# Performance work log

Hardware: AMD Instinct MI355X
Metric: run time of the kernel (lower is better)

Reference implementation:

```python
import jax, jax.numpy as jnp
import numpy as np

C, T, D = 32, 768, 100      # n_countries, n_times, n_ages (=n_features)
H = 5                        # attention heads (EncoderLayer default)
HID_GCN = 60                 # GCN hidden features
FFN = 64                     # feed_forward_dim
NPRED = 10                   # n_predictions
LHID = 200                   # hid_linear_part_dim
NL = 3                       # encoder layers


def setup_inputs() -> dict:
    key = jax.random.key(0)
    ks = jax.random.split(key, 24)
    s = 0.05
    rn = lambda k, shp: jax.random.normal(k, shp, jnp.float32) * s
    return {
        "X": jax.random.normal(ks[0], (C, T, D), jnp.float32),
        "A": jax.random.uniform(ks[1], (C, C), jnp.float32),
        # GCN params
        "gcn_w1": rn(ks[2], (D, HID_GCN)),
        "gcn_b1": rn(ks[3], (HID_GCN,)),
        "gcn_w2": rn(ks[4], (HID_GCN, D)),
        "gcn_b2": rn(ks[5], (D,)),
        # 3 stacked encoder layers
        "enc_wq": rn(ks[6], (NL, H, D, D)),
        "enc_wk": rn(ks[7], (NL, H, D, D)),
        "enc_wv": rn(ks[8], (NL, H, D, D)),
        "enc_wm": rn(ks[9], (NL, H * D, D)),
        "enc_f1w": rn(ks[10], (NL, D, FFN)),
        "enc_f1b": rn(ks[11], (NL, FFN)),
        "enc_f2w": rn(ks[12], (NL, FFN, D)),
        "enc_f2b": rn(ks[13], (NL, D)),
        "enc_ln1g": jnp.ones((NL, D), jnp.float32),
        "enc_ln1b": jnp.zeros((NL, D), jnp.float32),
        "enc_ln2g": jnp.ones((NL, D), jnp.float32),
        "enc_ln2b": jnp.zeros((NL, D), jnp.float32),
        "lin1_w": rn(ks[14], (D, LHID)),
        "lin1_b": rn(ks[15], (LHID,)),
        "lin2_w": rn(ks[16], (LHID, D)),
        "lin2_b": rn(ks[17], (D,)),
    }


def _layer_norm(x, g, b, eps=1e-5):
    m = x.mean(-1, keepdims=True)
    v = ((x - m) ** 2).mean(-1, keepdims=True)
    return (x - m) / jnp.sqrt(v + eps) * g + b


def _encoder_layer(x, wq, wk, wv, wm, f1w, f1b, f2w, f2b, g1, b1, g2, b2):
    # x: [C, T, D]; wq/wk/wv: [H, D, D]
    Q = jnp.einsum('ctd,hde->chte', x, wq)
    K = jnp.einsum('ctd,hde->chte', x, wk)
    V = jnp.einsum('ctd,hde->chte', x, wv)
    scores = jnp.einsum('chte,chse->chts', Q, K) / jnp.sqrt(jnp.float32(D))
    attn = jax.nn.softmax(scores, axis=-1)
    out = jnp.einsum('chts,chse->chte', attn, V)        # [C,H,T,D]
    out = out.transpose(0, 2, 1, 3).reshape(x.shape[0], x.shape[1], H * D)
    x = _layer_norm(x + out @ wm, g1, b1)
    ffn = jax.nn.relu(x @ f1w + f1b) @ f2w + f2b
    return _layer_norm(x + ffn, g2, b2)


def reference(X, A, gcn_w1, gcn_b1, gcn_w2, gcn_b2,
              enc_wq, enc_wk, enc_wv, enc_wm,
              enc_f1w, enc_f1b, enc_f2w, enc_f2b,
              enc_ln1g, enc_ln1b, enc_ln2g, enc_ln2b,
              lin1_w, lin1_b, lin2_w, lin2_b):
    n = A.shape[0]
    adj = A + jnp.eye(n, dtype=A.dtype)
    adj_hat = adj / adj.sum(-1, keepdims=True)
    # GCN layer 1
    h = jnp.einsum('ij,jta->ita', adj_hat, X)
    h = jnp.einsum('ita,ao->ito', h, gcn_w1) + gcn_b1
    h = jax.nn.relu(h)
    # GCN layer 2
    h = jnp.einsum('ij,jta->ita', adj_hat, h)
    h = jnp.einsum('ita,ao->ito', h, gcn_w2) + gcn_b2
    # 3 encoder layers (fixed structural loop)
    for l in range(NL):
        h = _encoder_layer(h, enc_wq[l], enc_wk[l], enc_wv[l], enc_wm[l],
                           enc_f1w[l], enc_f1b[l], enc_f2w[l], enc_f2b[l],
                           enc_ln1g[l], enc_ln1b[l], enc_ln2g[l], enc_ln2b[l])
    last = h[:, -1, :]  # [C, D]
    def step(carry, _):
        p = (carry @ lin1_w + lin1_b) @ lin2_w + lin2_b
        return p, p
    _, preds = jax.lax.scan(step, last, None, length=NPRED)  # [NPRED, C, D]
    return preds.transpose(1, 0, 2)  # [C, NPRED, D]
```

## Files before the change

### kernel.cpp

```cpp
#include <hip/hip_runtime.h>


#define ROWS 24576

#define OFF_ADJ   0L
#define OFF_X0    1024L
#define OFF_X1    (OFF_X0 + 2457600L)
#define OFF_XROW  (OFF_X1 + 3932160L)
#define OFF_XT    (OFF_XROW + 1572864L)
#define OFF_WBF   (OFF_XT + 1572864L)
#define OFF_MHT   (OFF_WBF + 6291456L)
#define OFF_USTT  (OFF_MHT + 122880L)
#define OFF_MP    (OFF_USTT + 98304L)
#define OFF_C0    (OFF_MP + 10000L)
#define OFF_F1WT  (OFF_C0 + 128L)
#define OFF_F2WT  (OFF_F1WT + 12288L)
#define OFF_GW1T  (OFF_F2WT + 10752L)
#define OFF_GW2T  (OFF_GW1T + 4096L)

typedef __attribute__((ext_vector_type(8))) short short8;
typedef __attribute__((ext_vector_type(4))) short short4v;
typedef __attribute__((ext_vector_type(4))) float float4v;
typedef __attribute__((ext_vector_type(2))) unsigned int uint2v;
typedef __attribute__((ext_vector_type(4))) unsigned int uint4v;

__device__ inline unsigned short f2bf(float f) {
    unsigned u = __builtin_bit_cast(unsigned, f);
    return (unsigned short)((u + 0x7fffu + ((u >> 16) & 1u)) >> 16);
}
__device__ inline unsigned pk2bf(float lo, float hi) {
    unsigned r;
    asm("v_cvt_pk_bf16_f32 %0, %1, %2" : "=v"(r) : "v"(lo), "v"(hi));
    return r;
}
__device__ inline void st4s(short* p, unsigned a, unsigned b) {
    *(short4v*)p = __builtin_bit_cast(short4v, (uint2v){a, b});
}
__device__ inline float bf2f(unsigned short v) {
    return __builtin_bit_cast(float, ((unsigned)v) << 16);
}
__device__ inline void gload16(const short* g, short* l) {
    __builtin_amdgcn_global_load_lds((const __attribute__((address_space(1))) void*)g,
                                     (__attribute__((address_space(3))) void*)l, 16, 0, 0);
}

__global__ void __launch_bounds__(256) k_mu2(const float* __restrict__ wq, const float* __restrict__ wk,
                                             const float* __restrict__ wv, const float* __restrict__ wm,
                                             const float* __restrict__ l1w, const float* __restrict__ l1b,
                                             const float* __restrict__ l2w, const float* __restrict__ l2b,
                                             const float* __restrict__ f1w, const float* __restrict__ f2w,
                                             const float* __restrict__ A,
                                             const float* __restrict__ gw1, const float* __restrict__ gw2,
                                             unsigned short* __restrict__ MhT, unsigned short* __restrict__ UstT,
                                             float* __restrict__ Mp, float* __restrict__ c0v,
                                             unsigned short* __restrict__ f1wT, unsigned short* __restrict__ f2wT,
                                             float* __restrict__ adjh,
                                             unsigned short* __restrict__ gw1T, unsigned short* __restrict__ gw2T) {
    int bi = blockIdx.x, tid = threadIdx.x;
    if (bi < 480) {
        int mat = bi >> 4, sub = bi & 15;
        int mode = mat / 15, idx = mat % 15, l = idx / 5, h = idx % 5;
        const float* Asrc = (mode == 0 ? wq : wv) + (l*5 + h)*10000;
        const float* Bsrc = (mode == 0) ? (wk + (l*5 + h)*10000) : (wm + l*50000 + h*10000);
        int oend = sub*625 + 625;
        for (int o = sub*625 + tid; o < oend; o += 256) {
            int r = o / 100, cix = o - (o/100)*100;
            const float* arow = Asrc + r*100;
            float acc = 0.f;
            if (mode == 0) {
                const float* brow = Bsrc + cix*100;
                for (int e = 0; e < 100; ++e) acc += arow[e] * brow[e];
                MhT[(long)(l*5 + h)*16384 + cix*128 + r] = f2bf(acc * 0.1f);
            } else {
                for (int e = 0; e < 100; ++e) acc += arow[e] * Bsrc[e*100 + cix];
                UstT[(long)l*65536 + (long)cix*512 + h*100 + r] = f2bf(acc);
            }
        }
        if (sub == 0) {
            if (mode == 0) {
                unsigned short* M0 = MhT + (long)(l*5 + h)*16384;
                for (int i = tid; i < 28*128; i += 256) M0[(100 + i/128)*128 + (i%128)] = 0;
                for (int i = tid; i < 100*28; i += 256) M0[(i/28)*128 + 100 + (i%28)] = 0;
            } else if (h == 4) {
                unsigned short* U0 = UstT + (long)l*65536;
                for (int i = tid; i < 28*512; i += 256) U0[(long)(100 + i/512)*512 + (i%512)] = 0;
                for (int i = tid; i < 100*12; i += 256) U0[(long)(i/12)*512 + 500 + (i%12)] = 0;
            }
        }
    } else if (bi < 496) {
        int sub = bi - 480;
        int oend = sub*625 + 625;
        for (int o = sub*625 + tid; o < oend; o += 256) {
            int r = o / 100, cix = o - (o/100)*100;
            const float* arow = l1w + r*200;
            float acc = 0.f;
            for (int e = 0; e < 200; ++e) acc += arow[e] * l2w[e*100 + cix];
            Mp[r*100 + cix] = acc;
        }
    } else if (bi == 496) {
        if (tid < 100) {
            float acc = l2b[tid];
            for (int e = 0; e < 200; ++e) acc += l1b[e] * l2w[e*100 + tid];
            c0v[tid] = acc;
        }
    } else if (bi < 500) {
        int l = bi - 497;
        unsigned short* F1 = f1wT + (long)l*8192;
        for (int i = tid; i < 8192; i += 256) {
            int o = i >> 7, k = i & 127;
            F1[i] = (k < 100) ? f2bf(f1w[l*6400 + k*64 + o]) : (unsigned short)0;
        }
        unsigned short* F2 = f2wT + (long)l*7168;
        for (int i = tid; i < 7168; i += 256) {
            int o2 = i >> 6, k2 = i & 63;
            F2[i] = (o2 < 100) ? f2bf(f2w[l*6400 + k2*100 + o2]) : (unsigned short)0;
        }
    } else if (bi == 500) {
        __shared__ float adj[1024];
        __shared__ float rs[32];
        for (int i = tid; i < 1024; i += 256) {
            int r = i >> 5, j = i & 31;
            adj[i] = A[i] + (r == j ? 1.f : 0.f);
        }
        __syncthreads();
        if (tid < 32) {
            float s = 0.f;
            #pragma unroll
            for (int jj = 0; jj < 32; ++jj) s += adj[tid*32 + jj];
            rs[tid] = s;
        }
        __syncthreads();
        for (int i = tid; i < 1024; i += 256) adjh[i] = adj[i] / rs[i >> 5];
    } else {
        for (int i = tid; i < 8192; i += 256) {
            int o = i >> 7, k = i & 127;
            gw1T[i] = (o < 60 && k < 100) ? f2bf(gw1[k*60 + o]) : (unsigned short)0;
        }
        for (int i = tid; i < 7168; i += 256) {
            int o = i >> 6, k = i & 63;
            gw2T[i] = (o < 100 && k < 60) ? f2bf(gw2[k*100 + o]) : (unsigned short)0;
        }
    }
}

__global__ void __launch_bounds__(128) k_gw1(const float* __restrict__ X,
                                             const unsigned short* __restrict__ gw1T,
                                             unsigned short* __restrict__ g) {
    const int tid = threadIdx.x, wave = tid >> 6, lane = tid & 63;
    const int l15 = lane & 15, l4 = lane >> 4;
    const long row = (long)blockIdx.x*32 + wave*16 + l15;
    const float* xrp = X + row*100;
    float4v acc[4];
    #pragma unroll
    for (int mt = 0; mt < 4; ++mt) acc[mt] = (float4v){0,0,0,0};
    #pragma unroll
    for (int ks = 0; ks < 4; ++ks) {
        short8 b;
        #pragma unroll
        for (int e = 0; e < 8; ++e) {
            int k = ks*32 + l4*8 + e;
            b[e] = (k < 100) ? (short)f2bf(xrp[k]) : (short)0;
        }
        #pragma unroll
        for (int mt = 0; mt < 4; ++mt) {
            short8 a = *(const short8*)((const short*)gw1T + (mt*16 + l15)*128 + ks*32 + l4*8);
            acc[mt] = __builtin_amdgcn_mfma_f32_16x16x32_bf16(a, b, acc[mt], 0, 0, 0);
        }
    }
    #pragma unroll
    for (int mt = 0; mt < 4; ++mt) {
        int o0 = mt*16 + l4*4;
        *(uint2v*)(g + row*64 + o0) =
            (uint2v){pk2bf(acc[mt][0], acc[mt][1]), pk2bf(acc[mt][2], acc[mt][3])};
    }
}

__global__ void __launch_bounds__(256) k_spmmg(const float* __restrict__ adjh,
                                               const unsigned short* __restrict__ g,
                                               const float* __restrict__ b1,
                                               unsigned short* __restrict__ hid) {
    __shared__ float adj[1024];
    int tid = threadIdx.x;
    for (int i = tid; i < 1024; i += 256) adj[i] = adjh[i];
    __syncthreads();
    long p = (long)blockIdx.x*256 + tid;
    int o = (int)(p & 63);
    float acc[32];
    #pragma unroll
    for (int i = 0; i < 32; ++i) acc[i] = 0.f;
    for (int j = 0; j < 32; ++j) {
        float xv = bf2f(g[(long)j*49152 + p]);
        #pragma unroll
        for (int i = 0; i < 32; ++i) acc[i] += adj[i*32 + j] * xv;
    }
    float bias = (o < 60) ? b1[o] : 0.f;
    #pragma unroll
    for (int i = 0; i < 32; ++i) hid[(long)i*49152 + p] = f2bf(fmaxf(acc[i] + bias, 0.f));
}

__global__ void __launch_bounds__(128) k_gw2(const unsigned short* __restrict__ hid,
                                             const unsigned short* __restrict__ gw2T,
                                             unsigned short* __restrict__ h2) {
    const int tid = threadIdx.x, wave = tid >> 6, lane = tid & 63;
    const int l15 = lane & 15, l4 = lane >> 4;
    const long row = (long)blockIdx.x*32 + wave*16 + l15;
    float4v acc[7];
    #pragma unroll
    for (int mt = 0; mt < 7; ++mt) acc[mt] = (float4v){0,0,0,0};
    #pragma unroll
    for (int ks = 0; ks < 2; ++ks) {
        short8 b = *(const short8*)((const short*)hid + row*64 + ks*32 + l4*8);
        #pragma unroll
        for (int mt = 0; mt < 7; ++mt) {
            short8 a = *(const short8*)((const short*)gw2T + (mt*16 + l15)*64 + ks*32 + l4*8);
            acc[mt] = __builtin_amdgcn_mfma_f32_16x16x32_bf16(a, b, acc[mt], 0, 0, 0);
        }
    }
    #pragma unroll
    for (int mt = 0; mt < 7; ++mt) {
        int o0 = mt*16 + l4*4;
        *(uint2v*)(h2 + row*128 + o0) =
            (uint2v){pk2bf(acc[mt][0], acc[mt][1]), pk2bf(acc[mt][2], acc[mt][3])};
    }
    *(uint2v*)(h2 + row*128 + 112 + l4*4) = (uint2v){0u, 0u};
}

__global__ void __launch_bounds__(384) k_spmmx(const float* __restrict__ adjh,
                                               const unsigned short* __restrict__ h2,
                                               const float* __restrict__ b2,
                                               float* __restrict__ x0,
                                               unsigned short* __restrict__ xrow,
                                               unsigned short* __restrict__ xT) {
    __shared__ float adj[1024];
    int tid = threadIdx.x;
    for (int i = tid; i < 1024; i += 384) adj[i] = adjh[i];
    __syncthreads();
    long p = (long)blockIdx.x*384 + tid;
    int o = (int)(p & 127);
    int t = (int)(p >> 7);
    float acc[32];
    #pragma unroll
    for (int i = 0; i < 32; ++i) acc[i] = 0.f;
    for (int j = 0; j < 32; ++j) {
        float xv = bf2f(h2[(long)j*98304 + p]);
        #pragma unroll
        for (int i = 0; i < 32; ++i) acc[i] += adj[i*32 + j] * xv;
    }
    if (o < 100) {
        float bias = b2[o];
        #pragma unroll
        for (int i = 0; i < 32; ++i) {
            float v = acc[i] + bias;
            x0[((long)i*768 + t)*100 + o] = v;
            unsigned short bv = f2bf(v);
            xrow[((long)i*768 + t)*128 + o] = bv;
            xT[(long)i*98304 + (long)o*768 + t] = bv;
        }
    } else {
        #pragma unroll
        for (int i = 0; i < 32; ++i) {
            xrow[((long)i*768 + t)*128 + o] = 0;
            if (o < 112) xT[(long)i*98304 + (long)o*768 + t] = 0;
        }
    }
}

__global__ void __launch_bounds__(256) k_attn12(const unsigned short* __restrict__ xrow,
                                                const unsigned short* __restrict__ xT,
                                                const unsigned short* __restrict__ MhT,
                                                unsigned short* __restrict__ Wb) {
    __shared__ __align__(16) short xr[2][64 * 128];
    __shared__ __align__(16) short xt[112 * 64];
    const int tid = threadIdx.x;
    const int wave = tid >> 6, lane = tid & 63;
    const int l15 = lane & 15, l4 = lane >> 4;
    const int c = blockIdx.z, h = blockIdx.y, q0 = blockIdx.x * 128;

    const short* xrg = (const short*)xrow + (long)c*768*128;
    const short* xtg = (const short*)xT + (long)c*128*768;
    const int rl4 = lane >> 4, cp16 = lane & 15;
    const int rl8 = lane >> 3, cp8 = lane & 7;
    const int njt = (wave == 3) ? 2 : 4;
    const int sw8 = (l15 & 7) << 3;
    const int swt = l15 & 7;

    #pragma unroll
    for (int j = 0; j < 4; ++j) {
        int row = wave*16 + j*4 + rl4;
        int lc = cp16 ^ (row & 7);
        gload16(xrg + (long)row*128 + lc*8, xr[0] + (wave*16 + j*4)*128);
    }

    short8 qb0[4], qb1[4];
    {
        short* mq = &xr[1][wave * 16 * 128];
        const short* Mb = (const short*)MhT + (long)h*16384 + l15*128 + l4*8;
        const short* xq = (const short*)xrow + ((long)c*768 + q0 + wave*16 + l15)*128 + l4*8;
        short8 bq0[4], bq1[4];
        #pragma unroll
        for (int kk = 0; kk < 4; ++kk) {
            bq0[kk] = *(const short8*)(xq + kk*32);
            bq1[kk] = *(const short8*)(xq + 64*128 + kk*32);
        }
        float4v qc0[8], qc1[8];
        #pragma unroll
        for (int mt = 0; mt < 8; ++mt) { qc0[mt] = (float4v){0,0,0,0}; qc1[mt] = (float4v){0,0,0,0}; }
        #pragma unroll
        for (int mt = 0; mt < 8; ++mt) {
            #pragma unroll
            for (int kk = 0; kk < 4; ++kk) {
                short8 a = *(const short8*)(Mb + (mt*16)*128 + kk*32);
                qc0[mt] = __builtin_amdgcn_mfma_f32_16x16x32_bf16(a, bq0[kk], qc0[mt], 0, 0, 0);
                qc1[mt] = __builtin_amdgcn_mfma_f32_16x16x32_bf16(a, bq1[kk], qc1[mt], 0, 0, 0);
            }
        }
        #pragma unroll
        for (int mt = 0; mt < 8; ++mt)
            st4s(mq + l15*128 + ((mt*16 + l4*4) ^ sw8),
                 pk2bf(qc0[mt][0], qc0[mt][1]), pk2bf(qc0[mt][2], qc0[mt][3]));
        asm volatile("" ::: "memory");
        #pragma unroll
        for (int kk = 0; kk < 4; ++kk)
            qb0[kk] = *(const short8*)(mq + l15*128 + ((kk*32 + l4*8) ^ sw8));
        asm volatile("" ::: "memory");
        #pragma unroll
        for (int mt = 0; mt < 8; ++mt)
            st4s(mq + l15*128 + ((mt*16 + l4*4) ^ sw8),
                 pk2bf(qc1[mt][0], qc1[mt][1]), pk2bf(qc1[mt][2], qc1[mt][3]));
        asm volatile("" ::: "memory");
        #pragma unroll
        for (int kk = 0; kk < 4; ++kk)
            qb1[kk] = *(const short8*)(mq + l15*128 + ((kk*32 + l4*8) ^ sw8));
    }

    __syncthreads();

    float4v o0[7], o1[7];
    #pragma unroll
    for (int n = 0; n < 7; ++n) { o0[n] = (float4v){0,0,0,0}; o1[n] = (float4v){0,0,0,0}; }
    float lsum0 = 0.f, lsum1 = 0.f;

    for (int kt = 0; kt < 12; ++kt) {
        const int key0 = kt * 64;
        const short* xrb = xr[kt & 1];

        for (int j = 0; j < njt; ++j) {
            int row = wave*32 + j*8 + rl8;
            int lc = cp8 ^ (row & 7);
            gload16(xtg + (long)row*768 + key0 + lc*8, xt + (wave*32 + j*8)*64);
        }
        if (kt < 11) {
            short* xrn = xr[(kt + 1) & 1];
            #pragma unroll
            for (int j = 0; j < 4; ++j) {
                int row = wave*16 + j*4 + rl4;
                int lc = cp16 ^ (row & 7);
                gload16(xrg + (long)(key0 + 64 + row)*128 + lc*8, xrn + (wave*16 + j*4)*128);
            }
        }
        __builtin_amdgcn_sched_barrier(0);

        unsigned pw0[4], pw1[4];
        #pragma unroll
        for (int kn = 0; kn < 2; ++kn) {
            float4v s0 = (float4v){0,0,0,0}, s1 = (float4v){0,0,0,0};
            #pragma unroll
            for (int kk = 0; kk < 4; ++kk) {
                short8 a = *(const short8*)(xrb + (kn*16 + l15)*128 + (((kk*4 + l4) ^ (l15 & 7))*8));
                s0 = __builtin_amdgcn_mfma_f32_16x16x32_bf16(a, qb0[kk], s0, 0, 0, 0);
                s1 = __builtin_amdgcn_mfma_f32_16x16x32_bf16(a, qb1[kk], s1, 0, 0, 0);
            }
            float p0[4], p1[4];
            #pragma unroll
            for (int r = 0; r < 4; ++r) {
                p0[r] = __expf(s0[r]); lsum0 += p0[r];
                p1[r] = __expf(s1[r]); lsum1 += p1[r];
            }
            pw0[kn*2]   = pk2bf(p0[0], p0[1]); pw0[kn*2+1] = pk2bf(p0[2], p0[3]);
            pw1[kn*2]   = pk2bf(p1[0], p1[1]); pw1[kn*2+1] = pk2bf(p1[2], p1[3]);
        }

        if (kt < 11) { asm volatile("s_waitcnt vmcnt(4)" ::: "memory"); }
        else         { asm volatile("s_waitcnt vmcnt(0)" ::: "memory"); }
        __builtin_amdgcn_s_barrier();

        {
            short8 b0 = __builtin_bit_cast(short8, (uint4v){pw0[0], pw0[1], pw0[2], pw0[3]});
            short8 b1 = __builtin_bit_cast(short8, (uint4v){pw1[0], pw1[1], pw1[2], pw1[3]});
            const int offLo = (((l4 >> 1) ^ swt) * 8) + (l4 & 1) * 4;
            const int offHi = (((2 + (l4 >> 1)) ^ swt) * 8) + (l4 & 1) * 4;
            #pragma unroll
            for (int dt = 0; dt < 7; ++dt) {
                const short* xrow_t = xt + (dt*16 + l15)*64;
                short4v lo = *(const short4v*)(xrow_t + offLo);
                short4v hi = *(const short4v*)(xrow_t + offHi);
                short8 a = __builtin_shufflevector(lo, hi, 0, 1, 2, 3, 4, 5, 6, 7);
                o0[dt] = __builtin_amdgcn_mfma_f32_16x16x32_bf16(a, b0, o0[dt], 0, 0, 0);
                o1[dt] = __builtin_amdgcn_mfma_f32_16x16x32_bf16(a, b1, o1[dt], 0, 0, 0);
            }
        }

        unsigned pw0b[4], pw1b[4];
        #pragma unroll
        for (int kn = 2; kn < 4; ++kn) {
            float4v s0 = (float4v){0,0,0,0}, s1 = (float4v){0,0,0,0};
            #pragma unroll
            for (int kk = 0; kk < 4; ++kk) {
                short8 a = *(const short8*)(xrb + (kn*16 + l15)*128 + (((kk*4 + l4) ^ (l15 & 7))*8));
                s0 = __builtin_amdgcn_mfma_f32_16x16x32_bf16(a, qb0[kk], s0, 0, 0, 0);
                s1 = __builtin_amdgcn_mfma_f32_16x16x32_bf16(a, qb1[kk], s1, 0, 0, 0);
            }
            float p0[4], p1[4];
            #pragma unroll
            for (int r = 0; r < 4; ++r) {
                p0[r] = __expf(s0[r]); lsum0 += p0[r];
                p1[r] = __expf(s1[r]); lsum1 += p1[r];
            }
            pw0b[(kn-2)*2]   = pk2bf(p0[0], p0[1]); pw0b[(kn-2)*2+1] = pk2bf(p0[2], p0[3]);
            pw1b[(kn-2)*2]   = pk2bf(p1[0], p1[1]); pw1b[(kn-2)*2+1] = pk2bf(p1[2], p1[3]);
        }

        {
            short8 b0 = __builtin_bit_cast(short8, (uint4v){pw0b[0], pw0b[1], pw0b[2], pw0b[3]});
            short8 b1 = __builtin_bit_cast(short8, (uint4v){pw1b[0], pw1b[1], pw1b[2], pw1b[3]});
            const int offLo = (((4 + (l4 >> 1)) ^ swt) * 8) + (l4 & 1) * 4;
            const int offHi = (((6 + (l4 >> 1)) ^ swt) * 8) + (l4 & 1) * 4;
            #pragma unroll
            for (int dt = 0; dt < 7; ++dt) {
                const short* xrow_t = xt + (dt*16 + l15)*64;
                short4v lo = *(const short4v*)(xrow_t + offLo);
                short4v hi = *(const short4v*)(xrow_t + offHi);
                short8 a = __builtin_shufflevector(lo, hi, 0, 1, 2, 3, 4, 5, 6, 7);
                o0[dt] = __builtin_amdgcn_mfma_f32_16x16x32_bf16(a, b0, o0[dt], 0, 0, 0);
                o1[dt] = __builtin_amdgcn_mfma_f32_16x16x32_bf16(a, b1, o1[dt], 0, 0, 0);
            }
        }
        __syncthreads();
    }

    float l0 = lsum0, l1 = lsum1;
    l0 += __shfl_xor(l0, 16, 64); l0 += __shfl_xor(l0, 32, 64);
    l1 += __shfl_xor(l1, 16, 64); l1 += __shfl_xor(l1, 32, 64);
    float inv0 = 1.f / l0, inv1 = 1.f / l1;

    unsigned short* Wo0 = Wb + ((long)(c*768 + q0 + wave*16 + l15))*512 + h*100 + l4*4;
    unsigned short* Wo1 = Wo0 + 64*512;
    #pragma unroll
    for (int dt = 0; dt < 7; ++dt) {
        if (dt < 6 || l4 == 0) {
            *(uint2v*)(Wo0 + dt*16) = (uint2v){pk2bf(o0[dt][0]*inv0, o0[dt][1]*inv0),
                                               pk2bf(o0[dt][2]*inv0, o0[dt][3]*inv0)};
            *(uint2v*)(Wo1 + dt*16) = (uint2v){pk2bf(o1[dt][0]*inv1, o1[dt][1]*inv1),
                                               pk2bf(o1[dt][2]*inv1, o1[dt][3]*inv1)};
        }
    }
    if (h == 0) {
        unsigned short* Wz = Wb + ((long)c*768 + q0)*512 + 500;
        for (int i = tid; i < 1536; i += 256) Wz[(long)(i/12)*512 + (i%12)] = 0;
    }
}

template<bool EMIT>
__global__ void __launch_bounds__(128) k_tail(const unsigned short* __restrict__ Wb,
        const unsigned short* __restrict__ UstT,
        const unsigned short* __restrict__ f1wT, const unsigned short* __restrict__ f2wT,
        const float* __restrict__ f1b, const float* __restrict__ f2b,
        const float* __restrict__ g1, const float* __restrict__ b1,
        const float* __restrict__ g2, const float* __restrict__ b2,
        float* __restrict__ x, unsigned short* __restrict__ xrow, unsigned short* __restrict__ xT) {
    __shared__ __align__(16) short ust[2][128 * 64];
    const int tid = threadIdx.x, wave = tid >> 6, lane = tid & 63;
    const int l15 = lane & 15, l4 = lane >> 4;
    const long row = (long)blockIdx.x*32 + wave*16 + l15;
    const int cc = blockIdx.x / 24;
    const int tt = (blockIdx.x % 24)*32 + wave*16 + l15;
    const int sr8 = lane >> 3, sc8 = lane & 7;

    const short* Wr = (const short*)Wb + row*512 + l4*8;
    float4v o[8];
    #pragma unroll
    for (int mt = 0; mt < 8; ++mt) o[mt] = (float4v){0,0,0,0};

    {
        short* dst = ust[0];
        #pragma unroll
        for (int j = 0; j < 8; ++j) {
            int r = wave*64 + j*8 + sr8;
            int lc = sc8 ^ (r & 7);
            gload16((const short*)UstT + (long)r*512 + 0 + lc*8, dst + (wave*64 + j*8)*64);
        }
    }
    __syncthreads();

    short8 bc0 = *(const short8*)(Wr + 0);
    short8 bc1 = *(const short8*)(Wr + 32);
    for (int cb = 0; cb < 8; ++cb) {
        if (cb < 7) {
            const int ksb = (cb + 1) * 64;
            short* dst = ust[(cb + 1) & 1];
            #pragma unroll
            for (int j = 0; j < 8; ++j) {
                int r = wave*64 + j*8 + sr8;
                int lc = sc8 ^ (r & 7);
                gload16((const short*)UstT + (long)r*512 + ksb + lc*8, dst + (wave*64 + j*8)*64);
            }
        }
        short8 bn0, bn1;
        if (cb < 7) {
            bn0 = *(const short8*)(Wr + (cb*2 + 2)*32);
            bn1 = *(const short8*)(Wr + (cb*2 + 3)*32);
        }
        __builtin_amdgcn_sched_barrier(0);

        const short* bufc = ust[cb & 1];
        #pragma unroll
        for (int mt = 0; mt < 8; ++mt) {
            short8 a0 = *(const short8*)(bufc + (mt*16 + l15)*64 + (((0*4 + l4) ^ (l15 & 7))*8));
            o[mt] = __builtin_amdgcn_mfma_f32_16x16x32_bf16(a0, bc0, o[mt], 0, 0, 0);
            short8 a1 = *(const short8*)(bufc + (mt*16 + l15)*64 + (((1*4 + l4) ^ (l15 & 7))*8));
            o[mt] = __builtin_amdgcn_mfma_f32_16x16x32_bf16(a1, bc1, o[mt], 0, 0, 0);
        }
        bc0 = bn0; bc1 = bn1;
        __syncthreads();
    }

    short* myz = ust[0] + wave * 2176;
    short* myt = ust[1] + wave * 1152;

    float zv[7][4];
    float sum = 0.f;
    #pragma unroll
    for (int mt = 0; mt < 7; ++mt) {
        int f0 = mt*16 + l4*4;
        float4 xv = {0,0,0,0};
        if (f0 < 100) xv = *(const float4*)(x + row*100 + f0);
        #pragma unroll
        for (int r = 0; r < 4; ++r) {
            float z = 0.f;
            if (f0 < 100) { z = o[mt][r] + ((const float*)&xv)[r]; sum += z; }
            zv[mt][r] = z;
        }
    }
    sum += __shfl_xor(sum, 16, 64); sum += __shfl_xor(sum, 32, 64);
    float mean = sum * 0.01f;
    float vs = 0.f;
    #pragma unroll
    for (int mt = 0; mt < 7; ++mt) {
        if (mt*16 + l4*4 < 100) {
            #pragma unroll
            for (int r = 0; r < 4; ++r) { float d = zv[mt][r] - mean; vs += d*d; }
        }
    }
    vs += __shfl_xor(vs, 16, 64); vs += __shfl_xor(vs, 32, 64);
    float inv = rsqrtf(vs * 0.01f + 1e-5f);
    float x1r[7][4];
    #pragma unroll
    for (int mt = 0; mt < 7; ++mt) {
        int f0 = mt*16 + l4*4;
        float4 gv = {0,0,0,0}, bv = {0,0,0,0};
        if (f0 < 100) { gv = *(const float4*)(g1 + f0); bv = *(const float4*)(b1 + f0); }
        #pragma unroll
        for (int r = 0; r < 4; ++r)
            x1r[mt][r] = (f0 < 100) ? (zv[mt][r] - mean) * inv * ((const float*)&gv)[r] + ((const float*)&bv)[r] : 0.f;
    }

    #pragma unroll
    for (int mt = 0; mt < 8; ++mt) {
        float v0 = (mt < 7) ? x1r[mt][0] : 0.f, v1 = (mt < 7) ? x1r[mt][1] : 0.f;
        float v2 = (mt < 7) ? x1r[mt][2] : 0.f, v3 = (mt < 7) ? x1r[mt][3] : 0.f;
        st4s(myz + l15*136 + mt*16 + l4*4, pk2bf(v0, v1), pk2bf(v2, v3));
    }
    asm volatile("" ::: "memory");

    float4v t2[4];
    #pragma unroll
    for (int m2t = 0; m2t < 4; ++m2t) t2[m2t] = (float4v){0,0,0,0};
    #pragma unroll
    for (int ks = 0; ks < 4; ++ks) {
        short8 b = *(const short8*)(myz + l15*136 + ks*32 + l4*8);
        #pragma unroll
        for (int m2t = 0; m2t < 4; ++m2t) {
            short8 a = *(const short8*)((const short*)f1wT + (m2t*16 + l15)*128 + ks*32 + l4*8);
            t2[m2t] = __builtin_amdgcn_mfma_f32_16x16x32_bf16(a, b, t2[m2t], 0, 0, 0);
        }
    }
    #pragma unroll
    for (int m2t = 0; m2t < 4; ++m2t) {
        int m20 = m2t*16 + l4*4;
        float4 bv = *(const float4*)(f1b + m20);
        float v0 = fmaxf(t2[m2t][0] + ((const float*)&bv)[0], 0.f);
        float v1 = fmaxf(t2[m2t][1] + ((const float*)&bv)[1], 0.f);
        float v2 = fmaxf(t2[m2t][2] + ((const float*)&bv)[2], 0.f);
        float v3 = fmaxf(t2[m2t][3] + ((const float*)&bv)[3], 0.f);
        st4s(myt + l15*72 + m20, pk2bf(v0, v1), pk2bf(v2, v3));
    }
    asm volatile("" ::: "memory");

    float4v o3[7];
    #pragma unroll
    for (int m3t = 0; m3t < 7; ++m3t) o3[m3t] = (float4v){0,0,0,0};
    #pragma unroll
    for (int ks2 = 0; ks2 < 2; ++ks2) {
        short8 b = *(const short8*)(myt + l15*72 + ks2*32 + l4*8);
        #pragma unroll
        for (int m3t = 0; m3t < 7; ++m3t) {
            short8 a = *(const short8*)((const short*)f2wT + (m3t*16 + l15)*64 + ks2*32 + l4*8);
            o3[m3t] = __builtin_amdgcn_mfma_f32_16x16x32_bf16(a, b, o3[m3t], 0, 0, 0);
        }
    }

    float z2[7][4];
    float sum2 = 0.f;
    #pragma unroll
    for (int m3t = 0; m3t < 7; ++m3t) {
        int f0 = m3t*16 + l4*4;
        float4 bv = {0,0,0,0};
        if (f0 < 100) bv = *(const float4*)(f2b + f0);
        #pragma unroll
        for (int r = 0; r < 4; ++r) {
            float z = 0.f;
            if (f0 < 100) { z = o3[m3t][r] + ((const float*)&bv)[r] + x1r[m3t][r]; sum2 += z; }
            z2[m3t][r] = z;
        }
    }
    sum2 += __shfl_xor(sum2, 16, 64); sum2 += __shfl_xor(sum2, 32, 64);
    float mean2 = sum2 * 0.01f;
    float vs2 = 0.f;
    #pragma unroll
    for (int m3t = 0; m3t < 7; ++m3t) {
        if (m3t*16 + l4*4 < 100) {
            #pragma unroll
            for (int r = 0; r < 4; ++r) { float d = z2[m3t][r] - mean2; vs2 += d*d; }
        }
    }
    vs2 += __shfl_xor(vs2, 16, 64); vs2 += __shfl_xor(vs2, 32, 64);
    float inv2 = rsqrtf(vs2 * 0.01f + 1e-5f);

    unsigned short* xTc = EMIT ? (xT + (long)cc*98304 + tt) : nullptr;
    #pragma unroll
    for (int m3t = 0; m3t < 7; ++m3t) {
        int f0 = m3t*16 + l4*4;
        if (f0 < 100) {
            float4 gv = *(const float4*)(g2 + f0);
            float4 bv = *(const float4*)(b2 + f0);
            float y[4];
            #pragma unroll
            for (int r = 0; r < 4; ++r)
                y[r] = (z2[m3t][r] - mean2) * inv2 * ((const float*)&gv)[r] + ((const float*)&bv)[r];
            *(float4*)(x + row*100 + f0) = (float4){y[0], y[1], y[2], y[3]};
            if (EMIT) {
                *(uint2v*)(xrow + row*128 + f0) = (uint2v){pk2bf(y[0], y[1]), pk2bf(y[2], y[3])};
                #pragma unroll
                for (int r = 0; r < 4; ++r)
                    xTc[(long)(f0 + r)*768] = f2bf(y[r]);
            }
        } else if (EMIT) {
            *(uint2v*)(xrow + row*128 + f0) = (uint2v){0u, 0u};
            #pragma unroll
            for (int r = 0; r < 4; ++r)
                if (f0 + r < 112) xTc[(long)(f0 + r)*768] = 0;
        }
    }
    if (EMIT) *(uint2v*)(xrow + row*128 + 112 + l4*4) = (uint2v){0u, 0u};
}

__global__ void __launch_bounds__(256) k_pred2(const float* __restrict__ xf,
        const float* __restrict__ Mp, const float* __restrict__ c0v,
        float* __restrict__ out) {
    int c = blockIdx.x, tid = threadIdx.x;
    __shared__ float Ml[10000];
    __shared__ float carry[100];
    for (int i = tid; i < 10000; i += 256) Ml[i] = Mp[i];
    if (tid < 100) carry[tid] = xf[((long)c*768 + 767)*100 + tid];
    __syncthreads();
    for (int s = 0; s < 10; ++s) {
        float pv = 0.f;
        if (tid < 100) {
            pv = c0v[tid];
            for (int d = 0; d < 100; ++d) pv += carry[d] * Ml[d*100 + tid];
            out[((long)c*10 + s)*100 + tid] = pv;
        }
        __syncthreads();
        if (tid < 100) carry[tid] = pv;
        __syncthreads();
    }
}

extern "C" void kernel_launch(void* const* d_in, const int* in_sizes, int n_in,
                              void* d_out, int out_size, void* d_ws, size_t ws_size,
                              hipStream_t stream) {
    const float* X    = (const float*)d_in[0];
    const float* A    = (const float*)d_in[1];
    const float* gw1  = (const float*)d_in[2];
    const float* gb1  = (const float*)d_in[3];
    const float* gw2  = (const float*)d_in[4];
    const float* gb2  = (const float*)d_in[5];
    const float* wq   = (const float*)d_in[6];
    const float* wk   = (const float*)d_in[7];
    const float* wv   = (const float*)d_in[8];
    const float* wm   = (const float*)d_in[9];
    const float* f1w  = (const float*)d_in[10];
    const float* f1b  = (const float*)d_in[11];
    const float* f2w  = (const float*)d_in[12];
    const float* f2b  = (const float*)d_in[13];
    const float* ln1g = (const float*)d_in[14];
    const float* ln1b = (const float*)d_in[15];
    const float* ln2g = (const float*)d_in[16];
    const float* ln2b = (const float*)d_in[17];
    const float* l1w  = (const float*)d_in[18];
    const float* l1b  = (const float*)d_in[19];
    const float* l2w  = (const float*)d_in[20];
    const float* l2b  = (const float*)d_in[21];
    (void)in_sizes; (void)n_in; (void)out_size; (void)ws_size;

    float* ws   = (float*)d_ws;
    float* adjh = ws + OFF_ADJ;
    float* x0   = ws + OFF_X0;
    unsigned short* gbuf = (unsigned short*)(ws + OFF_X1);
    unsigned short* hbuf = (unsigned short*)(ws + OFF_X1 + 786432L);
    unsigned short* h2buf= (unsigned short*)(ws + OFF_X1 + 1572864L);
    unsigned short* xrow = (unsigned short*)(ws + OFF_XROW);
    unsigned short* xTb  = (unsigned short*)(ws + OFF_XT);
    unsigned short* Wbf  = (unsigned short*)(ws + OFF_WBF);
    unsigned short* MhT  = (unsigned short*)(ws + OFF_MHT);
    unsigned short* UstT = (unsigned short*)(ws + OFF_USTT);
    float* Mp   = ws + OFF_MP;
    float* c0v  = ws + OFF_C0;
    unsigned short* f1wT = (unsigned short*)(ws + OFF_F1WT);
    unsigned short* f2wT = (unsigned short*)(ws + OFF_F2WT);
    unsigned short* gw1T = (unsigned short*)(ws + OFF_GW1T);
    unsigned short* gw2T = (unsigned short*)(ws + OFF_GW2T);
    float* out  = (float*)d_out;

    k_mu2<<<502, 256, 0, stream>>>(wq, wk, wv, wm, l1w, l1b, l2w, l2b, f1w, f2w, A, gw1, gw2,
                                   MhT, UstT, Mp, c0v, f1wT, f2wT, adjh, gw1T, gw2T);

    k_gw1<<<768, 128, 0, stream>>>(X, gw1T, gbuf);
    k_spmmg<<<192, 256, 0, stream>>>(adjh, gbuf, gb1, hbuf);
    k_gw2<<<768, 128, 0, stream>>>(hbuf, gw2T, h2buf);
    k_spmmx<<<256, 384, 0, stream>>>(adjh, h2buf, gb2, x0, xrow, xTb);

    for (int l = 0; l < 3; ++l) {
        k_attn12<<<dim3(6,5,32), 256, 0, stream>>>(xrow, xTb, MhT + (long)l*81920, Wbf);
        if (l < 2)
            k_tail<true><<<768, 128, 0, stream>>>(Wbf, UstT + (long)l*65536,
                f1wT + (long)l*8192, f2wT + (long)l*7168, f1b + l*64, f2b + l*100,
                ln1g + l*100, ln1b + l*100, ln2g + l*100, ln2b + l*100, x0, xrow, xTb);
        else
            k_tail<false><<<768, 128, 0, stream>>>(Wbf, UstT + (long)l*65536,
                f1wT + (long)l*8192, f2wT + (long)l*7168, f1b + l*64, f2b + l*100,
                ln1g + l*100, ln1b + l*100, ln2g + l*100, ln2b + l*100, x0, xrow, xTb);
    }

    k_pred2<<<32, 256, 0, stream>>>(x0, Mp, c0v, out);
}
```

Before: 466.6 us.

## Permute transposed activation layout to allow 16-byte LDS reads; add MFMA priority hints

The transposed bf16 activation buffer xT is now written with the time index permuted inside each 64-element block, in both producer kernels. The attention kernel's P·V MFMA operand can then be loaded as one contiguous short8 instead of two short4 loads joined by a shuffle. s_setprio is also raised around the MFMA-heavy loops in the attention and projection kernels so those waves get issue priority. The permutation must match the P fragment's key ordering exactly, so any mismatch would give wrong results.

Measured after the change: 461.7 us. Within noise of the previous version (-1.0%).

```diff
diff --git a/kernel.cpp b/kernel.cpp
--- a/kernel.cpp
+++ b/kernel.cpp
@@ -42,6 +42,11 @@
 __device__ inline void gload16(const short* g, short* l) {
     __builtin_amdgcn_global_load_lds((const __attribute__((address_space(1))) void*)g,
                                      (__attribute__((address_space(3))) void*)l, 16, 0, 0);
+}
+__device__ inline int permt(int t) {
+    int tl = t & 63, q = tl >> 2, r = tl & 3;
+    int pos = (q & 8) | ((q & 3) << 1) | ((q >> 2) & 1);
+    return (t & ~63) | (pos << 2) | r;
 }
 
 __global__ void __launch_bounds__(256) k_mu2(const float* __restrict__ wq, const float* __restrict__ wk,
@@ -238,6 +243,7 @@
     long p = (long)blockIdx.x*384 + tid;
     int o = (int)(p & 127);
     int t = (int)(p >> 7);
+    int tp = permt(t);
     float acc[32];
     #pragma unroll
     for (int i = 0; i < 32; ++i) acc[i] = 0.f;
@@ -254,13 +260,13 @@
             x0[((long)i*768 + t)*100 + o] = v;
             unsigned short bv = f2bf(v);
             xrow[((long)i*768 + t)*128 + o] = bv;
-            xT[(long)i*98304 + (long)o*768 + t] = bv;
+            xT[(long)i*98304 + (long)o*768 + tp] = bv;
         }
     } else {
         #pragma unroll
         for (int i = 0; i < 32; ++i) {
             xrow[((long)i*768 + t)*128 + o] = 0;
-            if (o < 112) xT[(long)i*98304 + (long)o*768 + t] = 0;
+            if (o < 112) xT[(long)i*98304 + (long)o*768 + tp] = 0;
         }
     }
 }
@@ -305,6 +311,7 @@
         float4v qc0[8], qc1[8];
         #pragma unroll
         for (int mt = 0; mt < 8; ++mt) { qc0[mt] = (float4v){0,0,0,0}; qc1[mt] = (float4v){0,0,0,0}; }
+        __builtin_amdgcn_s_setprio(1);
         #pragma unroll
         for (int mt = 0; mt < 8; ++mt) {
             #pragma unroll
@@ -314,6 +321,7 @@
                 qc1[mt] = __builtin_amdgcn_mfma_f32_16x16x32_bf16(a, bq1[kk], qc1[mt], 0, 0, 0);
             }
         }
+        __builtin_amdgcn_s_setprio(0);
         #pragma unroll
         for (int mt = 0; mt < 8; ++mt)
             st4s(mq + l15*128 + ((mt*16 + l4*4) ^ sw8),
@@ -361,6 +369,7 @@
         __builtin_amdgcn_sched_barrier(0);
 
         unsigned pw0[4], pw1[4];
+        __builtin_amdgcn_s_setprio(1);
         #pragma unroll
         for (int kn = 0; kn < 2; ++kn) {
             float4v s0 = (float4v){0,0,0,0}, s1 = (float4v){0,0,0,0};
@@ -379,22 +388,20 @@
             pw0[kn*2]   = pk2bf(p0[0], p0[1]); pw0[kn*2+1] = pk2bf(p0[2], p0[3]);
             pw1[kn*2]   = pk2bf(p1[0], p1[1]); pw1[kn*2+1] = pk2bf(p1[2], p1[3]);
         }
+        __builtin_amdgcn_s_setprio(0);
 
         if (kt < 11) { asm volatile("s_waitcnt vmcnt(4)" ::: "memory"); }
         else         { asm volatile("s_waitcnt vmcnt(0)" ::: "memory"); }
         __builtin_amdgcn_s_barrier();
 
+        __builtin_amdgcn_s_setprio(1);
         {
             short8 b0 = __builtin_bit_cast(short8, (uint4v){pw0[0], pw0[1], pw0[2], pw0[3]});
             short8 b1 = __builtin_bit_cast(short8, (uint4v){pw1[0], pw1[1], pw1[2], pw1[3]});
-            const int offLo = (((l4 >> 1) ^ swt) * 8) + (l4 & 1) * 4;
-            const int offHi = (((2 + (l4 >> 1)) ^ swt) * 8) + (l4 & 1) * 4;
+            const int offA = ((l4 ^ swt) * 8);
             #pragma unroll
             for (int dt = 0; dt < 7; ++dt) {
-                const short* xrow_t = xt + (dt*16 + l15)*64;
-                short4v lo = *(const short4v*)(xrow_t + offLo);
-                short4v hi = *(const short4v*)(xrow_t + offHi);
-                short8 a = __builtin_shufflevector(lo, hi, 0, 1, 2, 3, 4, 5, 6, 7);
+                short8 a = *(const short8*)(xt + (dt*16 + l15)*64 + offA);
                 o0[dt] = __builtin_amdgcn_mfma_f32_16x16x32_bf16(a, b0, o0[dt], 0, 0, 0);
                 o1[dt] = __builtin_amdgcn_mfma_f32_16x16x32_bf16(a, b1, o1[dt], 0, 0, 0);
             }
@@ -423,18 +430,15 @@
         {
             short8 b0 = __builtin_bit_cast(short8, (uint4v){pw0b[0], pw0b[1], pw0b[2], pw0b[3]});
             short8 b1 = __builtin_bit_cast(short8, (uint4v){pw1b[0], pw1b[1], pw1b[2], pw1b[3]});
-            const int offLo = (((4 + (l4 >> 1)) ^ swt) * 8) + (l4 & 1) * 4;
-            const int offHi = (((6 + (l4 >> 1)) ^ swt) * 8) + (l4 & 1) * 4;
+            const int offB = (((4 + l4) ^ swt) * 8);
             #pragma unroll
             for (int dt = 0; dt < 7; ++dt) {
-                const short* xrow_t = xt + (dt*16 + l15)*64;
-                short4v lo = *(const short4v*)(xrow_t + offLo);
-                short4v hi = *(const short4v*)(xrow_t + offHi);
-                short8 a = __builtin_shufflevector(lo, hi, 0, 1, 2, 3, 4, 5, 6, 7);
+                short8 a = *(const short8*)(xt + (dt*16 + l15)*64 + offB);
                 o0[dt] = __builtin_amdgcn_mfma_f32_16x16x32_bf16(a, b0, o0[dt], 0, 0, 0);
                 o1[dt] = __builtin_amdgcn_mfma_f32_16x16x32_bf16(a, b1, o1[dt], 0, 0, 0);
             }
         }
+        __builtin_amdgcn_s_setprio(0);
         __syncthreads();
     }
 
@@ -474,6 +478,7 @@
     const long row = (long)blockIdx.x*32 + wave*16 + l15;
     const int cc = blockIdx.x / 24;
     const int tt = (blockIdx.x % 24)*32 + wave*16 + l15;
+    const int ttp = permt(tt);
     const int sr8 = lane >> 3, sc8 = lane & 7;
 
     const short* Wr = (const short*)Wb + row*512 + l4*8;
@@ -513,6 +518,7 @@
         __builtin_amdgcn_sched_barrier(0);
 
         const short* bufc = ust[cb & 1];
+        __builtin_amdgcn_s_setprio(1);
         #pragma unroll
         for (int mt = 0; mt < 8; ++mt) {
             short8 a0 = *(const short8*)(bufc + (mt*16 + l15)*64 + (((0*4 + l4) ^ (l15 & 7))*8));
@@ -520,6 +526,7 @@
             short8 a1 = *(const short8*)(bufc + (mt*16 + l15)*64 + (((1*4 + l4) ^ (l15 & 7))*8));
             o[mt] = __builtin_amdgcn_mfma_f32_16x16x32_bf16(a1, bc1, o[mt], 0, 0, 0);
         }
+        __builtin_amdgcn_s_setprio(0);
         bc0 = bn0; bc1 = bn1;
         __syncthreads();
     }
@@ -636,7 +643,7 @@
     vs2 += __shfl_xor(vs2, 16, 64); vs2 += __shfl_xor(vs2, 32, 64);
     float inv2 = rsqrtf(vs2 * 0.01f + 1e-5f);
 
-    unsigned short* xTc = EMIT ? (xT + (long)cc*98304 + tt) : nullptr;
+    unsigned short* xTc = EMIT ? (xT + (long)cc*98304 + ttp) : nullptr;
     #pragma unroll
     for (int m3t = 0; m3t < 7; ++m3t) {
         int f0 = m3t*16 + l4*4;
```
